# Kernel optimization log

Hardware: AMD Instinct MI355X
Metric: run time of the kernel (lower is better)

Reference implementation:

```python
import jax, jax.numpy as jnp
import numpy as np

N = 100000
E = 1600000
IN_C = 128
HID = 256
K_EIG = 64
OUT_C = 16


def setup_inputs() -> dict:
    key = jax.random.key(0)
    ks = jax.random.split(key, 8)
    x = jax.random.normal(ks[0], (N, IN_C), dtype=jnp.float32)
    edge_index = jax.random.randint(ks[1], (2, E), 0, N)
    MLP_W = jax.random.normal(ks[2], (K_EIG, N), dtype=jnp.float32) * 0.02
    MLP_b = jax.random.normal(ks[3], (K_EIG,), dtype=jnp.float32) * 0.02
    mlpx_W = jax.random.normal(ks[4], (HID, IN_C), dtype=jnp.float32) * 0.05
    mlpx_b = jax.random.normal(ks[5], (HID,), dtype=jnp.float32) * 0.02
    fin_W = jax.random.normal(ks[6], (OUT_C, HID + K_EIG), dtype=jnp.float32) * 0.05
    fin_b = jax.random.normal(ks[7], (OUT_C,), dtype=jnp.float32) * 0.02
    return {"x": x, "edge_index": edge_index, "MLP_W": MLP_W, "MLP_b": MLP_b,
            "mlpx_W": mlpx_W, "mlpx_b": mlpx_b, "fin_W": fin_W, "fin_b": fin_b}


def _spmm(row, col, feats, n):
    # adj is COO with coords (col[e], row[e]) and value 1 -> out[col] += feats[row]
    return jax.ops.segment_sum(feats[row], col, num_segments=n)


def _pump(xA, row, col, n):
    # MinCut-style pump: soft assignment, normalized-cut loss + orthogonality loss
    S = jax.nn.softmax(xA, axis=-1)                      # [N, K]
    AS = _spmm(row, col, S, n)                            # A @ S, [N, K]
    cut = jnp.sum(S * AS)                                 # tr(S^T A S)
    deg = jax.ops.segment_sum(jnp.ones(col.shape, S.dtype), col, num_segments=n)
    deg_term = jnp.sum(deg[:, None] * S * S)              # tr(S^T D S)
    pump_loss = -(cut / deg_term)
    SS = S.T @ S                                          # [K, K]
    k = S.shape[1]
    ortho_loss = jnp.linalg.norm(SS / jnp.linalg.norm(SS)
                                 - jnp.eye(k, dtype=S.dtype) / jnp.sqrt(jnp.asarray(k, S.dtype)))
    return S, pump_loss, ortho_loss


def reference(x, edge_index, MLP_W, MLP_b, mlpx_W, mlpx_b, fin_W, fin_b):
    row, col = edge_index[0], edge_index[1]
    n = x.shape[0]
    # xA = adj @ MLP.weight.T + bias   (irregular gather/scatter over edges)
    xA = _spmm(row, col, MLP_W.T, n) + MLP_b              # [N, K]
    xX = x @ mlpx_W.T + mlpx_b                            # [N, HID]
    xA, pump_loss, ortho_loss = _pump(xA, row, col, n)
    z = jnp.concatenate([xX, xA], axis=1)                 # [N, HID+K]
    # dropout omitted (eval mode)
    z = jax.nn.log_softmax(z @ fin_W.T + fin_b, axis=-1)  # [N, OUT]
    return (z, pump_loss + ortho_loss)
```

## Files before the change

kernel.cpp:

```cpp
#include <hip/hip_runtime.h>
#include <math.h>

#define N_NODES 100000
#define N_EDGES 1600000
#define IN_C    128
#define HID     256
#define KEIG    64
#define OUT_C   16

#define NPB      256
#define NBUCKET  ((N_NODES + NPB - 1) / NPB)
#define EDGE_TILE 4096
#define NTILE    ((N_EDGES + EDGE_TILE - 1) / EDGE_TILE)

#define TRANS_BLOCKS   ((N_NODES + 63) / 64)
#define GATHER_BLOCKS  2048
#define CUT_BLOCKS     2048
#define SSP_BLOCKS     512
#define OUT_BLOCKS     ((N_NODES + 255) / 256)

typedef __attribute__((ext_vector_type(8))) short short8;
typedef __attribute__((ext_vector_type(4))) float f32x4;

__device__ __forceinline__ float wave_sum(float v) {
#pragma unroll
    for (int m = 32; m; m >>= 1) v += __shfl_xor(v, m, 64);
    return v;
}
__device__ __forceinline__ float wave_max(float v) {
#pragma unroll
    for (int m = 32; m; m >>= 1) v = fmaxf(v, __shfl_xor(v, m, 64));
    return v;
}
__device__ __forceinline__ float bf2f(unsigned int u) {
    return __uint_as_float((u & 0xffffu) << 16);
}
__device__ __forceinline__ unsigned short f2bf(float f) {
    unsigned int u = __float_as_uint(f);
    u += 0x7fff + ((u >> 16) & 1);
    return (unsigned short)(u >> 16);
}
__device__ __forceinline__ float fp8tof(int b) {
    return __builtin_amdgcn_cvt_f32_fp8(b, 0);
}
__device__ __forceinline__ unsigned char f2fp8(float f) {
    int p = __builtin_amdgcn_cvt_pk_fp8_f32(f, f, 0, false);
    return (unsigned char)(p & 0xff);
}

#define FMA4(P, s, W) \
    P.x = fmaf(s, W.x, P.x); P.y = fmaf(s, W.y, P.y); \
    P.z = fmaf(s, W.z, P.z); P.w = fmaf(s, W.w, P.w);

__global__ void prep_weff(const float* __restrict__ mlpxW, const float* __restrict__ mlpxb,
                          const float* __restrict__ finW, const float* __restrict__ finb,
                          float* __restrict__ Weff, float* __restrict__ beff,
                          int* __restrict__ bcnt) {
    int t = blockIdx.x * blockDim.x + threadIdx.x;
    const int NW = (IN_C + KEIG) * OUT_C;
    if (t < NW) {
        int k = t >> 4, o = t & 15;
        float acc;
        if (k < IN_C) {
            acc = 0.f;
            for (int c = 0; c < HID; ++c)
                acc += mlpxW[c * IN_C + k] * finW[o * (HID + KEIG) + c];
        } else {
            acc = finW[o * (HID + KEIG) + HID + (k - IN_C)];
        }
        Weff[k * OUT_C + o] = acc;
    }
    int tb = t - NW;
    if (tb >= 0 && tb < OUT_C) {
        float acc = finb[tb];
        for (int c = 0; c < HID; ++c) acc += mlpxb[c] * finW[tb * (HID + KEIG) + c];
        beff[tb] = acc;
    }
    int tz = t - (NW + OUT_C);
    if (tz >= 0 && tz <= NBUCKET) bcnt[tz] = 0;
}

__global__ void transpose_w(const float* __restrict__ W, unsigned char* __restrict__ WT8) {
    __shared__ float tile[64][65];
    int n0 = blockIdx.x * 64;
    int t = threadIdx.x;
    int tn = t & 63, tq = t >> 6;
#pragma unroll
    for (int kk = 0; kk < 16; ++kk) {
        int k = tq * 16 + kk;
        int n = n0 + tn;
        tile[k][tn] = (n < N_NODES) ? W[(long long)k * N_NODES + n] : 0.f;
    }
    __syncthreads();
    int tk = t & 63;
#pragma unroll
    for (int ii = 0; ii < 16; ++ii) {
        int n = n0 + tq * 16 + ii;
        if (n < N_NODES) WT8[(unsigned)n * 64u + tk] = f2fp8(tile[tk][tq * 16 + ii] * 32.f);
    }
}

__global__ void bucket_hist(const int* __restrict__ ei, int* __restrict__ bcnt) {
    __shared__ int h[NBUCKET];
    int t = threadIdx.x;
    for (int i = t; i < NBUCKET; i += 256) h[i] = 0;
    __syncthreads();
    int e0 = blockIdx.x * EDGE_TILE;
    int e1 = min(e0 + EDGE_TILE, N_EDGES);
    for (int e = e0 + t; e < e1; e += 256)
        atomicAdd(&h[ei[N_EDGES + e] >> 8], 1);
    __syncthreads();
    for (int i = t; i < NBUCKET; i += 256)
        if (h[i]) atomicAdd(&bcnt[i], h[i]);
}

__global__ void bucket_scan(const int* __restrict__ bcnt, int* __restrict__ bbase,
                            int* __restrict__ bcur) {
    __shared__ int sh[512];
    int t = threadIdx.x;
    int v = (t < NBUCKET) ? bcnt[t] : 0;
    sh[t] = v;
    __syncthreads();
    for (int d = 1; d < 512; d <<= 1) {
        int u = (t >= d) ? sh[t - d] : 0;
        __syncthreads();
        sh[t] += u;
        __syncthreads();
    }
    if (t < NBUCKET) { bbase[t] = sh[t] - v; bcur[t] = sh[t] - v; }
    if (t == 0) bbase[NBUCKET] = N_EDGES;
}

__global__ void bucket_scatter(const int* __restrict__ ei, int* __restrict__ bcur,
                               int* __restrict__ ebuf) {
    __shared__ int h[NBUCKET];
    __shared__ int gb[NBUCKET];
    int t = threadIdx.x;
    for (int i = t; i < NBUCKET; i += 256) h[i] = 0;
    __syncthreads();
    int e0 = blockIdx.x * EDGE_TILE;
    int e1 = min(e0 + EDGE_TILE, N_EDGES);
    for (int e = e0 + t; e < e1; e += 256)
        atomicAdd(&h[ei[N_EDGES + e] >> 8], 1);
    __syncthreads();
    for (int i = t; i < NBUCKET; i += 256) {
        int c = h[i];
        gb[i] = c ? atomicAdd(&bcur[i], c) : 0;
        h[i] = 0;
    }
    __syncthreads();
    for (int e = e0 + t; e < e1; e += 256) {
        int r = ei[e];
        int c = ei[N_EDGES + e];
        int b = c >> 8;
        int pos = gb[b] + atomicAdd(&h[b], 1);
        ebuf[pos] = r | ((c & 255) << 17);
    }
}

__global__ void csr_build(const int* __restrict__ ebuf, const int* __restrict__ bbase,
                          int* __restrict__ offsets, int* __restrict__ csr_row) {
    __shared__ int hist[NPB];
    __shared__ int sh[NPB];
    __shared__ int curs[NPB];
    int b = blockIdx.x;
    int t = threadIdx.x;
    int s0 = bbase[b], s1 = bbase[b + 1];
    hist[t] = 0;
    __syncthreads();
    for (int i = s0 + t; i < s1; i += 256)
        atomicAdd(&hist[ebuf[i] >> 17], 1);
    __syncthreads();
    int v = hist[t];
    sh[t] = v;
    __syncthreads();
    for (int d = 1; d < 256; d <<= 1) {
        int u = (t >= d) ? sh[t - d] : 0;
        __syncthreads();
        sh[t] += u;
        __syncthreads();
    }
    int excl = s0 + sh[t] - v;
    int node = b * NPB + t;
    if (node < N_NODES) offsets[node] = excl;
    curs[t] = excl;
    __syncthreads();
    for (int i = s0 + t; i < s1; i += 256) {
        int pk = ebuf[i];
        int pos = atomicAdd(&curs[pk >> 17], 1);
        csr_row[pos] = pk & 0x1FFFF;
    }
    if (b == 0 && t == 0) offsets[N_NODES] = N_EDGES;
}

__global__ void gather_softmax(const int* __restrict__ offsets, const int* __restrict__ csr_row,
                               const unsigned char* __restrict__ WT8,
                               const float* __restrict__ MLPb,
                               unsigned short* __restrict__ Sb,
                               unsigned char* __restrict__ S8,
                               float* __restrict__ dtp) {
    int lane = threadIdx.x & 63;
    int wib = __builtin_amdgcn_readfirstlane(threadIdx.x >> 6);
    int gw = blockIdx.x * 4 + wib;
    int nw = gridDim.x * 4;
    float bias = MLPb[lane];
    float dacc = 0.f;
    for (int n = gw; n < N_NODES; n += nw) {
        int s0 = __builtin_amdgcn_readfirstlane(offsets[n]);
        int s1 = __builtin_amdgcn_readfirstlane(offsets[n + 1]);
        float acc = 0.f;
        int j = s0;
        for (; j + 7 < s1; j += 8) {
            int r0 = csr_row[j + 0], r1 = csr_row[j + 1];
            int r2 = csr_row[j + 2], r3 = csr_row[j + 3];
            int r4 = csr_row[j + 4], r5 = csr_row[j + 5];
            int r6 = csr_row[j + 6], r7 = csr_row[j + 7];
            int b0 = WT8[(unsigned)r0 * 64u + lane];
            int b1 = WT8[(unsigned)r1 * 64u + lane];
            int b2 = WT8[(unsigned)r2 * 64u + lane];
            int b3 = WT8[(unsigned)r3 * 64u + lane];
            int b4 = WT8[(unsigned)r4 * 64u + lane];
            int b5 = WT8[(unsigned)r5 * 64u + lane];
            int b6 = WT8[(unsigned)r6 * 64u + lane];
            int b7 = WT8[(unsigned)r7 * 64u + lane];
            acc += ((fp8tof(b0) + fp8tof(b1)) + (fp8tof(b2) + fp8tof(b3)))
                 + ((fp8tof(b4) + fp8tof(b5)) + (fp8tof(b6) + fp8tof(b7)));
        }
        for (; j < s1; ++j)
            acc += fp8tof(WT8[(unsigned)csr_row[j] * 64u + lane]);
        acc = bias + acc * 0.03125f;
        float m = wave_max(acc);
        float e = __expf(acc - m);
        float sm = wave_sum(e);
        float sv = e / sm;
        unsigned idx = (unsigned)n * 64u + lane;
        Sb[idx] = f2bf(sv);
        S8[idx] = f2fp8(sv * 64.f);
        dacc += (float)(s1 - s0) * sv * sv;
    }
    dacc = wave_sum(dacc);
    __shared__ float red[4];
    if (lane == 0) red[wib] = dacc;
    __syncthreads();
    if (threadIdx.x == 0) dtp[blockIdx.x] = red[0] + red[1] + red[2] + red[3];
}

__global__ void cut_csr(const int* __restrict__ offsets, const int* __restrict__ csr_row,
                        const unsigned short* __restrict__ Sb,
                        const unsigned char* __restrict__ S8, float* __restrict__ cutp) {
    int lane = threadIdx.x & 63;
    int wib = __builtin_amdgcn_readfirstlane(threadIdx.x >> 6);
    int gw = blockIdx.x * 4 + wib;
    int nw = gridDim.x * 4;
    float acc = 0.f;
    for (int n = gw; n < N_NODES; n += nw) {
        float sc = bf2f(Sb[(unsigned)n * 64u + lane]);
        int s0 = __builtin_amdgcn_readfirstlane(offsets[n]);
        int s1 = __builtin_amdgcn_readfirstlane(offsets[n + 1]);
        float g = 0.f;
        int j = s0;
        for (; j + 7 < s1; j += 8) {
            int r0 = csr_row[j + 0], r1 = csr_row[j + 1];
            int r2 = csr_row[j + 2], r3 = csr_row[j + 3];
            int r4 = csr_row[j + 4], r5 = csr_row[j + 5];
            int r6 = csr_row[j + 6], r7 = csr_row[j + 7];
            int b0 = S8[(unsigned)r0 * 64u + lane];
            int b1 = S8[(unsigned)r1 * 64u + lane];
            int b2 = S8[(unsigned)r2 * 64u + lane];
            int b3 = S8[(unsigned)r3 * 64u + lane];
            int b4 = S8[(unsigned)r4 * 64u + lane];
            int b5 = S8[(unsigned)r5 * 64u + lane];
            int b6 = S8[(unsigned)r6 * 64u + lane];
            int b7 = S8[(unsigned)r7 * 64u + lane];
            g += ((fp8tof(b0) + fp8tof(b1)) + (fp8tof(b2) + fp8tof(b3)))
               + ((fp8tof(b4) + fp8tof(b5)) + (fp8tof(b6) + fp8tof(b7)));
        }
        for (; j < s1; ++j)
            g += fp8tof(S8[(unsigned)csr_row[j] * 64u + lane]);
        acc += sc * g * 0.015625f;
    }
    acc = wave_sum(acc);
    __shared__ float red[4];
    if (lane == 0) red[wib] = acc;
    __syncthreads();
    if (threadIdx.x == 0) cutp[blockIdx.x] = red[0] + red[1] + red[2] + red[3];
}

__global__ __launch_bounds__(256) void ss_mfma(const unsigned short* __restrict__ Sb,
                                               float* __restrict__ ssp) {
    __shared__ unsigned short Sr[32][66];
    int t = threadIdx.x;
    int lane = t & 63;
    int w = t >> 6;
    int m = lane & 15;
    int quad = lane >> 4;
    int srow = t >> 3;
    int spart = t & 7;

    f32x4 a0 = {0.f,0.f,0.f,0.f}, a1 = {0.f,0.f,0.f,0.f};
    f32x4 a2 = {0.f,0.f,0.f,0.f}, a3 = {0.f,0.f,0.f,0.f};

    for (int base = blockIdx.x * 32; base < N_NODES; base += SSP_BLOCKS * 32) {
        const uint4* g = (const uint4*)(Sb + (long long)(base + srow) * 64 + spart * 8);
        uint4 d = *g;
        __syncthreads();
        unsigned int* rowp = (unsigned int*)&Sr[srow][0];
        rowp[spart * 4 + 0] = d.x;
        rowp[spart * 4 + 1] = d.y;
        rowp[spart * 4 + 2] = d.z;
        rowp[spart * 4 + 3] = d.w;
        __syncthreads();

        short8 f0, f1, f2, f3;
#pragma unroll
        for (int j = 0; j < 8; ++j) {
            int k = quad * 8 + j;
            f0[j] = (short)Sr[k][m];
            f1[j] = (short)Sr[k][16 + m];
            f2[j] = (short)Sr[k][32 + m];
            f3[j] = (short)Sr[k][48 + m];
        }
        short8 fa = (w == 0) ? f0 : (w == 1) ? f1 : (w == 2) ? f2 : f3;
        a0 = __builtin_amdgcn_mfma_f32_16x16x32_bf16(fa, f0, a0, 0, 0, 0);
        a1 = __builtin_amdgcn_mfma_f32_16x16x32_bf16(fa, f1, a1, 0, 0, 0);
        a2 = __builtin_amdgcn_mfma_f32_16x16x32_bf16(fa, f2, a2, 0, 0, 0);
        a3 = __builtin_amdgcn_mfma_f32_16x16x32_bf16(fa, f3, a3, 0, 0, 0);
    }

    float* dst = ssp + (size_t)blockIdx.x * 4096;
#pragma unroll
    for (int r = 0; r < 4; ++r) {
        int row = w * 16 + quad * 4 + r;
        dst[row * 64 +  0 + m] = a0[r];
        dst[row * 64 + 16 + m] = a1[r];
        dst[row * 64 + 32 + m] = a2[r];
        dst[row * 64 + 48 + m] = a3[r];
    }
}

__global__ void reduce_ss(const float* __restrict__ ssp, float* __restrict__ SS) {
    int e = blockIdx.x * blockDim.x + threadIdx.x;
    float s = 0.f;
    for (int p = 0; p < SSP_BLOCKS; ++p) s += ssp[(size_t)p * 4096 + e];
    SS[e] = s;
}

__global__ void scalars_kernel(const float* __restrict__ cutp, const float* __restrict__ dtp,
                               const float* __restrict__ SS, float* __restrict__ out) {
    __shared__ float red[256];
    int t = threadIdx.x;
    float c = 0.f;
    for (int i = t; i < CUT_BLOCKS; i += 256) c += cutp[i];
    red[t] = c; __syncthreads();
    for (int s = 128; s; s >>= 1) { if (t < s) red[t] += red[t + s]; __syncthreads(); }
    float cut = red[0]; __syncthreads();

    float d = 0.f;
    for (int i = t; i < GATHER_BLOCKS; i += 256) d += dtp[i];
    red[t] = d; __syncthreads();
    for (int s = 128; s; s >>= 1) { if (t < s) red[t] += red[t + s]; __syncthreads(); }
    float dterm = red[0]; __syncthreads();

    float ss[16];
    float sq = 0.f;
#pragma unroll
    for (int j = 0; j < 16; ++j) { ss[j] = SS[t * 16 + j]; sq += ss[j] * ss[j]; }
    red[t] = sq; __syncthreads();
    for (int s = 128; s; s >>= 1) { if (t < s) red[t] += red[t + s]; __syncthreads(); }
    float nrm = sqrtf(red[0]); __syncthreads();

    float osq = 0.f;
#pragma unroll
    for (int j = 0; j < 16; ++j) {
        int idx = t * 16 + j;
        float v = ss[j] / nrm - ((idx % 65 == 0) ? 0.125f : 0.f);
        osq += v * v;
    }
    red[t] = osq; __syncthreads();
    for (int s = 128; s; s >>= 1) { if (t < s) red[t] += red[t + s]; __syncthreads(); }
    if (t == 0) {
        float loss = -(cut / dterm) + sqrtf(red[0]);
        out[(long long)N_NODES * OUT_C] = loss;
    }
}

__global__ __launch_bounds__(256) void out_kernel(const float* __restrict__ x,
                           const unsigned short* __restrict__ Sb,
                           const float* __restrict__ Weff, const float* __restrict__ beff,
                           float* __restrict__ out) {
    __shared__ float4 Wsh[192 * 4];
    __shared__ float bsh[16];
    int t = threadIdx.x;
    const float4* W4 = (const float4*)Weff;
    for (int i = t; i < 768; i += 256) Wsh[i] = W4[i];
    if (t < 16) bsh[t] = beff[t];
    __syncthreads();

    int r = blockIdx.x * 256 + t;
    if (r >= N_NODES) return;

    float4 p0 = make_float4(bsh[0], bsh[1], bsh[2], bsh[3]);
    float4 p1 = make_float4(bsh[4], bsh[5], bsh[6], bsh[7]);
    float4 p2 = make_float4(bsh[8], bsh[9], bsh[10], bsh[11]);
    float4 p3 = make_float4(bsh[12], bsh[13], bsh[14], bsh[15]);

    const float4* xr = (const float4*)(x + (long long)r * IN_C);
#pragma unroll 8
    for (int j = 0; j < 32; ++j) {
        float4 xv = xr[j];
        int k = j * 4;
        float xs[4] = {xv.x, xv.y, xv.z, xv.w};
#pragma unroll
        for (int c = 0; c < 4; ++c) {
            float s = xs[c];
            float4 w0 = Wsh[(k + c) * 4 + 0];
            float4 w1 = Wsh[(k + c) * 4 + 1];
            float4 w2 = Wsh[(k + c) * 4 + 2];
            float4 w3 = Wsh[(k + c) * 4 + 3];
            FMA4(p0, s, w0); FMA4(p1, s, w1); FMA4(p2, s, w2); FMA4(p3, s, w3);
        }
    }
    const uint2* sr = (const uint2*)(Sb + (long long)r * 64);
#pragma unroll 8
    for (int j = 0; j < 16; ++j) {
        uint2 u = sr[j];
        float xs[4] = {bf2f(u.x), bf2f(u.x >> 16), bf2f(u.y), bf2f(u.y >> 16)};
        int k = IN_C + j * 4;
#pragma unroll
        for (int c = 0; c < 4; ++c) {
            float s = xs[c];
            float4 w0 = Wsh[(k + c) * 4 + 0];
            float4 w1 = Wsh[(k + c) * 4 + 1];
            float4 w2 = Wsh[(k + c) * 4 + 2];
            float4 w3 = Wsh[(k + c) * 4 + 3];
            FMA4(p0, s, w0); FMA4(p1, s, w1); FMA4(p2, s, w2); FMA4(p3, s, w3);
        }
    }

    float m = fmaxf(fmaxf(fmaxf(p0.x, p0.y), fmaxf(p0.z, p0.w)),
                    fmaxf(fmaxf(fmaxf(p1.x, p1.y), fmaxf(p1.z, p1.w)),
                          fmaxf(fmaxf(fmaxf(p2.x, p2.y), fmaxf(p2.z, p2.w)),
                                fmaxf(fmaxf(p3.x, p3.y), fmaxf(p3.z, p3.w)))));
    float sum = __expf(p0.x - m) + __expf(p0.y - m) + __expf(p0.z - m) + __expf(p0.w - m)
              + __expf(p1.x - m) + __expf(p1.y - m) + __expf(p1.z - m) + __expf(p1.w - m)
              + __expf(p2.x - m) + __expf(p2.y - m) + __expf(p2.z - m) + __expf(p2.w - m)
              + __expf(p3.x - m) + __expf(p3.y - m) + __expf(p3.z - m) + __expf(p3.w - m);
    float lse = m + logf(sum);
    float4* o4 = (float4*)(out + (long long)r * OUT_C);
    o4[0] = make_float4(p0.x - lse, p0.y - lse, p0.z - lse, p0.w - lse);
    o4[1] = make_float4(p1.x - lse, p1.y - lse, p1.z - lse, p1.w - lse);
    o4[2] = make_float4(p2.x - lse, p2.y - lse, p2.z - lse, p2.w - lse);
    o4[3] = make_float4(p3.x - lse, p3.y - lse, p3.z - lse, p3.w - lse);
}

extern "C" void kernel_launch(void* const* d_in, const int* in_sizes, int n_in,
                              void* d_out, int out_size, void* d_ws, size_t ws_size,
                              hipStream_t stream) {
    const float* x     = (const float*)d_in[0];
    const int*   ei    = (const int*)d_in[1];
    const float* MLPW  = (const float*)d_in[2];
    const float* MLPb  = (const float*)d_in[3];
    const float* mlpxW = (const float*)d_in[4];
    const float* mlpxb = (const float*)d_in[5];
    const float* finW  = (const float*)d_in[6];
    const float* finb  = (const float*)d_in[7];
    float* out = (float*)d_out;
    char* ws = (char*)d_ws;

    unsigned char*  WT8 = (unsigned char*)ws;
    unsigned short* Sb  = (unsigned short*)(ws + (size_t)N_NODES * 64);
    unsigned char*  S8  = (unsigned char*)(ws + (size_t)N_NODES * 192);
    float* ssp  = (float*)(ws + (size_t)N_NODES * 256);
    float* SS   = ssp + (size_t)SSP_BLOCKS * 4096;
    float* Weff = SS + 4096;
    float* beff = Weff + 192 * 16;
    float* cutp = beff + 16;
    float* dtp  = cutp + CUT_BLOCKS;
    int* ebuf    = (int*)(dtp + GATHER_BLOCKS);
    int* csr_row = ebuf + N_EDGES;
    int* offsets = csr_row + N_EDGES;
    int* bcnt    = offsets + N_NODES + 1;
    int* bbase   = bcnt + NBUCKET + 1;
    int* bcur    = bbase + NBUCKET + 1;

    hipLaunchKernelGGL(prep_weff, dim3(14), dim3(256), 0, stream,
                       mlpxW, mlpxb, finW, finb, Weff, beff, bcnt);
    hipLaunchKernelGGL(transpose_w, dim3(TRANS_BLOCKS), dim3(256), 0, stream, MLPW, WT8);
    hipLaunchKernelGGL(bucket_hist, dim3(NTILE), dim3(256), 0, stream, ei, bcnt);
    hipLaunchKernelGGL(bucket_scan, dim3(1), dim3(512), 0, stream, bcnt, bbase, bcur);
    hipLaunchKernelGGL(bucket_scatter, dim3(NTILE), dim3(256), 0, stream, ei, bcur, ebuf);
    hipLaunchKernelGGL(csr_build, dim3(NBUCKET), dim3(256), 0, stream,
                       ebuf, bbase, offsets, csr_row);
    hipLaunchKernelGGL(gather_softmax, dim3(GATHER_BLOCKS), dim3(256), 0, stream,
                       offsets, csr_row, WT8, MLPb, Sb, S8, dtp);
    hipLaunchKernelGGL(cut_csr, dim3(CUT_BLOCKS), dim3(256), 0, stream,
                       offsets, csr_row, Sb, S8, cutp);
    hipLaunchKernelGGL(ss_mfma, dim3(SSP_BLOCKS), dim3(256), 0, stream, Sb, ssp);
    hipLaunchKernelGGL(reduce_ss, dim3(16), dim3(256), 0, stream, ssp, SS);
    hipLaunchKernelGGL(scalars_kernel, dim3(1), dim3(256), 0, stream, cutp, dtp, SS, out);
    hipLaunchKernelGGL(out_kernel, dim3(OUT_BLOCKS), dim3(256), 0, stream, x, Sb, Weff, beff, out);
}
```

Baseline: 330.6 us.

## Pad CSR rows to multiples of eight and stage scatters in shared memory

```diff
diff --git a/kernel.cpp b/kernel.cpp
--- a/kernel.cpp
+++ b/kernel.cpp
@@ -12,6 +12,7 @@
 #define NBUCKET  ((N_NODES + NPB - 1) / NPB)
 #define EDGE_TILE 4096
 #define NTILE    ((N_EDGES + EDGE_TILE - 1) / EDGE_TILE)
+#define CAP      7168
 
 #define TRANS_BLOCKS   ((N_NODES + 63) / 64)
 #define GATHER_BLOCKS  2048
@@ -55,7 +56,8 @@
 __global__ void prep_weff(const float* __restrict__ mlpxW, const float* __restrict__ mlpxb,
                           const float* __restrict__ finW, const float* __restrict__ finb,
                           float* __restrict__ Weff, float* __restrict__ beff,
-                          int* __restrict__ bcnt) {
+                          int* __restrict__ bcnt, unsigned char* __restrict__ WT8,
+                          unsigned char* __restrict__ S8, int* __restrict__ gpad) {
     int t = blockIdx.x * blockDim.x + threadIdx.x;
     const int NW = (IN_C + KEIG) * OUT_C;
     if (t < NW) {
@@ -78,6 +80,12 @@
     }
     int tz = t - (NW + OUT_C);
     if (tz >= 0 && tz <= NBUCKET) bcnt[tz] = 0;
+    int tp = t - (NW + OUT_C + NBUCKET + 1);
+    if (tp >= 0 && tp < 16) {
+        ((int*)(WT8 + (size_t)N_NODES * 64))[tp] = 0;
+        ((int*)(S8 + (size_t)N_NODES * 64))[tp] = 0;
+        if (tp == 0) *gpad = 0;
+    }
 }
 
 __global__ void transpose_w(const float* __restrict__ W, unsigned char* __restrict__ WT8) {
@@ -135,34 +143,62 @@
                                int* __restrict__ ebuf) {
     __shared__ int h[NBUCKET];
     __shared__ int gb[NBUCKET];
+    __shared__ int lpre[NBUCKET];
+    __shared__ int psum[256];
+    __shared__ int stage[EDGE_TILE];
+    __shared__ short bkt[EDGE_TILE];
     int t = threadIdx.x;
     for (int i = t; i < NBUCKET; i += 256) h[i] = 0;
     __syncthreads();
     int e0 = blockIdx.x * EDGE_TILE;
     int e1 = min(e0 + EDGE_TILE, N_EDGES);
+    int nt = e1 - e0;
     for (int e = e0 + t; e < e1; e += 256)
         atomicAdd(&h[ei[N_EDGES + e] >> 8], 1);
+    __syncthreads();
+    int a0 = (2 * t < NBUCKET) ? h[2 * t] : 0;
+    int a1 = (2 * t + 1 < NBUCKET) ? h[2 * t + 1] : 0;
+    psum[t] = a0 + a1;
+    __syncthreads();
+    for (int d = 1; d < 256; d <<= 1) {
+        int u = (t >= d) ? psum[t - d] : 0;
+        __syncthreads();
+        psum[t] += u;
+        __syncthreads();
+    }
+    int base = (t == 0) ? 0 : psum[t - 1];
+    if (2 * t < NBUCKET) lpre[2 * t] = base;
+    if (2 * t + 1 < NBUCKET) lpre[2 * t + 1] = base + a0;
     __syncthreads();
     for (int i = t; i < NBUCKET; i += 256) {
         int c = h[i];
         gb[i] = c ? atomicAdd(&bcur[i], c) : 0;
-        h[i] = 0;
+        h[i] = lpre[i];
     }
     __syncthreads();
     for (int e = e0 + t; e < e1; e += 256) {
         int r = ei[e];
         int c = ei[N_EDGES + e];
         int b = c >> 8;
-        int pos = gb[b] + atomicAdd(&h[b], 1);
-        ebuf[pos] = r | ((c & 255) << 17);
+        int slot = atomicAdd(&h[b], 1);
+        stage[slot] = r | ((c & 255) << 17);
+        bkt[slot] = (short)b;
+    }
+    __syncthreads();
+    for (int s = t; s < nt; s += 256) {
+        int b = bkt[s];
+        ebuf[gb[b] + s - lpre[b]] = stage[s];
     }
 }
 
 __global__ void csr_build(const int* __restrict__ ebuf, const int* __restrict__ bbase,
-                          int* __restrict__ offsets, int* __restrict__ csr_row) {
+                          int* __restrict__ offsets, int* __restrict__ pstart,
+                          int* __restrict__ csr_row, int* __restrict__ gpad) {
     __shared__ int hist[NPB];
     __shared__ int sh[NPB];
     __shared__ int curs[NPB];
+    __shared__ int staged[CAP];
+    __shared__ int pbase_sh;
     int b = blockIdx.x;
     int t = threadIdx.x;
     int s0 = bbase[b], s1 = bbase[b + 1];
@@ -172,7 +208,8 @@
         atomicAdd(&hist[ebuf[i] >> 17], 1);
     __syncthreads();
     int v = hist[t];
-    sh[t] = v;
+    int pv = (v + 7) & ~7;
+    sh[t] = pv;
     __syncthreads();
     for (int d = 1; d < 256; d <<= 1) {
         int u = (t >= d) ? sh[t - d] : 0;
@@ -180,20 +217,38 @@
         sh[t] += u;
         __syncthreads();
     }
-    int excl = s0 + sh[t] - v;
+    int pexcl = sh[t] - pv;
+    int pt = sh[255];
+    if (t == 0) pbase_sh = atomicAdd(gpad, pt);
+    __syncthreads();
+    int pbase = pbase_sh;
     int node = b * NPB + t;
-    if (node < N_NODES) offsets[node] = excl;
-    curs[t] = excl;
-    __syncthreads();
-    for (int i = s0 + t; i < s1; i += 256) {
-        int pk = ebuf[i];
-        int pos = atomicAdd(&curs[pk >> 17], 1);
-        csr_row[pos] = pk & 0x1FFFF;
-    }
-    if (b == 0 && t == 0) offsets[N_NODES] = N_EDGES;
-}
-
-__global__ void gather_softmax(const int* __restrict__ offsets, const int* __restrict__ csr_row,
+    if (node < N_NODES) { offsets[node] = v; pstart[node] = pbase + pexcl; }
+    curs[t] = pexcl;
+    __syncthreads();
+    if (pt <= CAP) {
+        for (int i = t; i < pt; i += 256) staged[i] = N_NODES;
+        __syncthreads();
+        for (int i = s0 + t; i < s1; i += 256) {
+            int pk = ebuf[i];
+            int pos = atomicAdd(&curs[pk >> 17], 1);
+            staged[pos] = pk & 0x1FFFF;
+        }
+        __syncthreads();
+        for (int i = t; i < pt; i += 256) csr_row[pbase + i] = staged[i];
+    } else {
+        for (int i = t; i < pt; i += 256) csr_row[pbase + i] = N_NODES;
+        __syncthreads();
+        for (int i = s0 + t; i < s1; i += 256) {
+            int pk = ebuf[i];
+            int pos = atomicAdd(&curs[pk >> 17], 1);
+            csr_row[pbase + pos] = pk & 0x1FFFF;
+        }
+    }
+}
+
+__global__ void gather_softmax(const int* __restrict__ offsets, const int* __restrict__ pstart,
+                               const int* __restrict__ csr_row,
                                const unsigned char* __restrict__ WT8,
                                const float* __restrict__ MLPb,
                                unsigned short* __restrict__ Sb,
@@ -206,15 +261,15 @@
     float bias = MLPb[lane];
     float dacc = 0.f;
     for (int n = gw; n < N_NODES; n += nw) {
-        int s0 = __builtin_amdgcn_readfirstlane(offsets[n]);
-        int s1 = __builtin_amdgcn_readfirstlane(offsets[n + 1]);
+        int deg = __builtin_amdgcn_readfirstlane(offsets[n]);
+        int ps  = __builtin_amdgcn_readfirstlane(pstart[n]);
+        int plen = (deg + 7) & ~7;
         float acc = 0.f;
-        int j = s0;
-        for (; j + 7 < s1; j += 8) {
-            int r0 = csr_row[j + 0], r1 = csr_row[j + 1];
-            int r2 = csr_row[j + 2], r3 = csr_row[j + 3];
-            int r4 = csr_row[j + 4], r5 = csr_row[j + 5];
-            int r6 = csr_row[j + 6], r7 = csr_row[j + 7];
+        for (int j = 0; j < plen; j += 8) {
+            int r0 = csr_row[ps + j + 0], r1 = csr_row[ps + j + 1];
+            int r2 = csr_row[ps + j + 2], r3 = csr_row[ps + j + 3];
+            int r4 = csr_row[ps + j + 4], r5 = csr_row[ps + j + 5];
+            int r6 = csr_row[ps + j + 6], r7 = csr_row[ps + j + 7];
             int b0 = WT8[(unsigned)r0 * 64u + lane];
             int b1 = WT8[(unsigned)r1 * 64u + lane];
             int b2 = WT8[(unsigned)r2 * 64u + lane];
@@ -226,8 +281,6 @@
             acc += ((fp8tof(b0) + fp8tof(b1)) + (fp8tof(b2) + fp8tof(b3)))
                  + ((fp8tof(b4) + fp8tof(b5)) + (fp8tof(b6) + fp8tof(b7)));
         }
-        for (; j < s1; ++j)
-            acc += fp8tof(WT8[(unsigned)csr_row[j] * 64u + lane]);
         acc = bias + acc * 0.03125f;
         float m = wave_max(acc);
         float e = __expf(acc - m);
@@ -236,7 +289,7 @@
         unsigned idx = (unsigned)n * 64u + lane;
         Sb[idx] = f2bf(sv);
         S8[idx] = f2fp8(sv * 64.f);
-        dacc += (float)(s1 - s0) * sv * sv;
+        dacc += (float)deg * sv * sv;
     }
     dacc = wave_sum(dacc);
     __shared__ float red[4];
@@ -245,7 +298,8 @@
     if (threadIdx.x == 0) dtp[blockIdx.x] = red[0] + red[1] + red[2] + red[3];
 }
 
-__global__ void cut_csr(const int* __restrict__ offsets, const int* __restrict__ csr_row,
+__global__ void cut_csr(const int* __restrict__ offsets, const int* __restrict__ pstart,
+                        const int* __restrict__ csr_row,
                         const unsigned short* __restrict__ Sb,
                         const unsigned char* __restrict__ S8, float* __restrict__ cutp) {
     int lane = threadIdx.x & 63;
@@ -255,15 +309,15 @@
     float acc = 0.f;
     for (int n = gw; n < N_NODES; n += nw) {
         float sc = bf2f(Sb[(unsigned)n * 64u + lane]);
-        int s0 = __builtin_amdgcn_readfirstlane(offsets[n]);
-        int s1 = __builtin_amdgcn_readfirstlane(offsets[n + 1]);
+        int deg = __builtin_amdgcn_readfirstlane(offsets[n]);
+        int ps  = __builtin_amdgcn_readfirstlane(pstart[n]);
+        int plen = (deg + 7) & ~7;
         float g = 0.f;
-        int j = s0;
-        for (; j + 7 < s1; j += 8) {
-            int r0 = csr_row[j + 0], r1 = csr_row[j + 1];
-            int r2 = csr_row[j + 2], r3 = csr_row[j + 3];
-            int r4 = csr_row[j + 4], r5 = csr_row[j + 5];
-            int r6 = csr_row[j + 6], r7 = csr_row[j + 7];
+        for (int j = 0; j < plen; j += 8) {
+            int r0 = csr_row[ps + j + 0], r1 = csr_row[ps + j + 1];
+            int r2 = csr_row[ps + j + 2], r3 = csr_row[ps + j + 3];
+            int r4 = csr_row[ps + j + 4], r5 = csr_row[ps + j + 5];
+            int r6 = csr_row[ps + j + 6], r7 = csr_row[ps + j + 7];
             int b0 = S8[(unsigned)r0 * 64u + lane];
             int b1 = S8[(unsigned)r1 * 64u + lane];
             int b2 = S8[(unsigned)r2 * 64u + lane];
@@ -275,8 +329,6 @@
             g += ((fp8tof(b0) + fp8tof(b1)) + (fp8tof(b2) + fp8tof(b3)))
                + ((fp8tof(b4) + fp8tof(b5)) + (fp8tof(b6) + fp8tof(b7)));
         }
-        for (; j < s1; ++j)
-            g += fp8tof(S8[(unsigned)csr_row[j] * 64u + lane]);
         acc += sc * g * 0.015625f;
     }
     acc = wave_sum(acc);
@@ -468,9 +520,10 @@
     char* ws = (char*)d_ws;
 
     unsigned char*  WT8 = (unsigned char*)ws;
-    unsigned short* Sb  = (unsigned short*)(ws + (size_t)N_NODES * 64);
-    unsigned char*  S8  = (unsigned char*)(ws + (size_t)N_NODES * 192);
-    float* ssp  = (float*)(ws + (size_t)N_NODES * 256);
+    unsigned char*  S8  = (unsigned char*)(ws + (size_t)(N_NODES + 1) * 64);
+    unsigned short* Sb  = (unsigned short*)(ws + (size_t)(N_NODES + 1) * 128);
+    char* p = ws + (size_t)(N_NODES + 1) * 128 + (size_t)N_NODES * 128;
+    float* ssp  = (float*)p;
     float* SS   = ssp + (size_t)SSP_BLOCKS * 4096;
     float* Weff = SS + 4096;
     float* beff = Weff + 192 * 16;
@@ -478,23 +531,25 @@
     float* dtp  = cutp + CUT_BLOCKS;
     int* ebuf    = (int*)(dtp + GATHER_BLOCKS);
     int* csr_row = ebuf + N_EDGES;
-    int* offsets = csr_row + N_EDGES;
-    int* bcnt    = offsets + N_NODES + 1;
+    int* offsets = csr_row + N_EDGES + 8 * ((N_NODES + NPB - 1) / NPB) * NPB + 8 * N_NODES;
+    int* pstart  = offsets + N_NODES + 1;
+    int* bcnt    = pstart + N_NODES;
     int* bbase   = bcnt + NBUCKET + 1;
     int* bcur    = bbase + NBUCKET + 1;
-
-    hipLaunchKernelGGL(prep_weff, dim3(14), dim3(256), 0, stream,
-                       mlpxW, mlpxb, finW, finb, Weff, beff, bcnt);
+    int* gpad    = bcur + NBUCKET;
+
+    hipLaunchKernelGGL(prep_weff, dim3(16), dim3(256), 0, stream,
+                       mlpxW, mlpxb, finW, finb, Weff, beff, bcnt, WT8, S8, gpad);
     hipLaunchKernelGGL(transpose_w, dim3(TRANS_BLOCKS), dim3(256), 0, stream, MLPW, WT8);
     hipLaunchKernelGGL(bucket_hist, dim3(NTILE), dim3(256), 0, stream, ei, bcnt);
     hipLaunchKernelGGL(bucket_scan, dim3(1), dim3(512), 0, stream, bcnt, bbase, bcur);
     hipLaunchKernelGGL(bucket_scatter, dim3(NTILE), dim3(256), 0, stream, ei, bcur, ebuf);
     hipLaunchKernelGGL(csr_build, dim3(NBUCKET), dim3(256), 0, stream,
-                       ebuf, bbase, offsets, csr_row);
+                       ebuf, bbase, offsets, pstart, csr_row, gpad);
     hipLaunchKernelGGL(gather_softmax, dim3(GATHER_BLOCKS), dim3(256), 0, stream,
-                       offsets, csr_row, WT8, MLPb, Sb, S8, dtp);
+                       offsets, pstart, csr_row, WT8, MLPb, Sb, S8, dtp);
     hipLaunchKernelGGL(cut_csr, dim3(CUT_BLOCKS), dim3(256), 0, stream,
-                       offsets, csr_row, Sb, S8, cutp);
+                       offsets, pstart, csr_row, Sb, S8, cutp);
     hipLaunchKernelGGL(ss_mfma, dim3(SSP_BLOCKS), dim3(256), 0, stream, Sb, ssp);
     hipLaunchKernelGGL(reduce_ss, dim3(16), dim3(256), 0, stream, ssp, SS);
     hipLaunchKernelGGL(scalars_kernel, dim3(1), dim3(256), 0, stream, cutp, dtp, SS, out);
```

New measurement: 308.5 us. -6.7%, faster.
